# Kernel optimization log

Hardware: AMD Instinct MI355X
Metric: run time of the kernel (lower is better)

The kernel has to match this reference:

```python
import jax, jax.numpy as jnp
import numpy as np

N, NODE_DIM, EDGE_DIM, E, H, L, G = 100000, 128, 16, 1200000, 64, 3, 1000


def gcn_conv(x, w, b, row, col, dis):
    # PyG GCNConv: x @ W, symmetric-normalized aggregation with self-loops, + bias
    xw = x @ w                                    # [N, H]
    norm = dis[row] * dis[col]                    # [E]
    msg = norm[:, None] * xw[row]                 # [E, H]
    out = jax.ops.segment_sum(msg, col, num_segments=N)
    out = out + (dis * dis)[:, None] * xw         # self-loop contribution
    return out + b


def reference(x, edge_attr, node_w, node_b, edge_w, edge_b, conv_w, conv_b,
              cls_w1, cls_b1, cls_w2, cls_b2, edge_index, batch, num_graphs):
    row, col = edge_index[0], edge_index[1]
    # node embed
    h = x @ node_w + node_b                       # [N, H]
    # edge embed aggregated to both endpoints
    e = edge_attr @ edge_w + edge_b               # [E, H]
    edge_aggr = jax.ops.segment_sum(e, row, num_segments=N) \
              + jax.ops.segment_sum(e, col, num_segments=N)
    h = h + edge_aggr
    # degree with self-loops (deg over col, matching PyG GCNConv default flow)
    deg = jax.ops.segment_sum(jnp.ones((E,), h.dtype), col, num_segments=N) + 1.0
    dis = jnp.where(deg > 0, jax.lax.rsqrt(deg), 0.0)
    xs = []
    for i in range(L):
        h = jax.nn.relu(gcn_conv(h, conv_w[i], conv_b[i], row, col, dis))
        xs.append(h)
    hj = jnp.concatenate(xs, axis=-1)             # JumpingKnowledge 'cat' -> [N, L*H]
    # global mean pool over batch index
    sums = jax.ops.segment_sum(hj, batch, num_segments=num_graphs)
    cnts = jax.ops.segment_sum(jnp.ones((N,), hj.dtype), batch, num_segments=num_graphs)
    pooled = sums / jnp.maximum(cnts, 1.0)[:, None]  # [G, L*H]
    # classifier (eval mode: dropout is identity)
    z = jax.nn.relu(pooled @ cls_w1 + cls_b1)
    out = z @ cls_w2 + cls_b2                     # [G, 1]
    return out.squeeze(-1)


def setup_inputs() -> dict:
    key = jax.random.key(0)
    ks = jax.random.split(key, 16)
    s = lambda fan: 1.0 / np.sqrt(fan)
    return {
        "x": jax.random.normal(ks[0], (N, NODE_DIM), jnp.float32),
        "edge_attr": jax.random.normal(ks[1], (E, EDGE_DIM), jnp.float32),
        "node_w": jax.random.uniform(ks[2], (NODE_DIM, H), jnp.float32, -s(NODE_DIM), s(NODE_DIM)),
        "node_b": jnp.zeros((H,), jnp.float32),
        "edge_w": jax.random.uniform(ks[3], (EDGE_DIM, H), jnp.float32, -s(EDGE_DIM), s(EDGE_DIM)),
        "edge_b": jnp.zeros((H,), jnp.float32),
        "conv_w": jax.random.uniform(ks[4], (L, H, H), jnp.float32, -s(H), s(H)),
        "conv_b": jnp.zeros((L, H), jnp.float32),
        "cls_w1": jax.random.uniform(ks[5], (L * H, H // 2), jnp.float32, -s(L * H), s(L * H)),
        "cls_b1": jnp.zeros((H // 2,), jnp.float32),
        "cls_w2": jax.random.uniform(ks[6], (H // 2, 1), jnp.float32, -s(H // 2), s(H // 2)),
        "cls_b2": jnp.zeros((1,), jnp.float32),
        "edge_index": jax.random.randint(ks[7], (2, E), 0, N, jnp.int64 if jax.config.jax_enable_x64 else jnp.int32),
        "batch": jnp.sort(jax.random.randint(ks[8], (N,), 0, G, jnp.int64 if jax.config.jax_enable_x64 else jnp.int32)),
        "num_graphs": G,
    }
```

## Files before the change

kernel.cpp:

```cpp
#include <hip/hip_runtime.h>
#include <math.h>


#define EPB 4096

__global__ __launch_bounds__(256) void k_embed(
    const float* __restrict__ x, const float* __restrict__ w,
    const float* __restrict__ b, float* __restrict__ out, int N) {
  __shared__ __align__(16) float rl[64 * 128];
  const int t = threadIdx.x;
  const int j = t & 63;
  const int wv = t >> 6;
  const int base = blockIdx.x * 64;
  float wr[128];
#pragma unroll
  for (int k = 0; k < 128; ++k) wr[k] = w[k * 64 + j];
  const float bj = b[j];
#pragma unroll
  for (int it = 0; it < 8; ++it) {
    int lin = (t + it * 256) * 4;
    int r = lin >> 7, c = lin & 127;
    int row = base + r;
    float4 v = (row < N) ? *(const float4*)&x[(size_t)row * 128 + c]
                         : make_float4(0.f, 0.f, 0.f, 0.f);
    *(float4*)&rl[lin] = v;
  }
  __syncthreads();
  for (int r = wv; r < 64; r += 4) {
    int row = base + r;
    if (row >= N) break;
    float acc = bj;
#pragma unroll
    for (int k4 = 0; k4 < 32; ++k4) {
      float4 a = *(const float4*)&rl[r * 128 + k4 * 4];
      acc = fmaf(a.x, wr[k4 * 4 + 0], acc);
      acc = fmaf(a.y, wr[k4 * 4 + 1], acc);
      acc = fmaf(a.z, wr[k4 * 4 + 2], acc);
      acc = fmaf(a.w, wr[k4 * 4 + 3], acc);
    }
    out[(size_t)row * 64 + j] = acc;
  }
}

__global__ __launch_bounds__(256) void k_conv(
    const float* __restrict__ hin, const float* __restrict__ w,
    const float* __restrict__ dis, float* __restrict__ xws, int N) {
  __shared__ __align__(16) float rl[64 * 64];
  const int t = threadIdx.x;
  const int j = t & 63;
  const int wv = t >> 6;
  const int base = blockIdx.x * 64;
  float wr[64];
#pragma unroll
  for (int k = 0; k < 64; ++k) wr[k] = w[k * 64 + j];
#pragma unroll
  for (int it = 0; it < 4; ++it) {
    int lin = (t + it * 256) * 4;
    int r = lin >> 6, c = lin & 63;
    int row = base + r;
    float4 v = (row < N) ? *(const float4*)&hin[(size_t)row * 64 + c]
                         : make_float4(0.f, 0.f, 0.f, 0.f);
    *(float4*)&rl[lin] = v;
  }
  __syncthreads();
  for (int r = wv; r < 64; r += 4) {
    int row = base + r;
    if (row >= N) break;
    float acc = 0.f;
#pragma unroll
    for (int k4 = 0; k4 < 16; ++k4) {
      float4 a = *(const float4*)&rl[r * 64 + k4 * 4];
      acc = fmaf(a.x, wr[k4 * 4 + 0], acc);
      acc = fmaf(a.y, wr[k4 * 4 + 1], acc);
      acc = fmaf(a.z, wr[k4 * 4 + 2], acc);
      acc = fmaf(a.w, wr[k4 * 4 + 3], acc);
    }
    xws[(size_t)row * 64 + j] = dis[row] * acc;
  }
}

__global__ __launch_bounds__(256) void k_hist(
    const int* __restrict__ erow, const int* __restrict__ ecol,
    int* __restrict__ matTc, int* __restrict__ matTr, int E, int NB, int NBLK) {
  __shared__ int hc[512], hr[512];
  int b = blockIdx.x, t = threadIdx.x;
  for (int i = t; i < NB; i += 256) { hc[i] = 0; hr[i] = 0; }
  __syncthreads();
  int e0 = b * EPB;
#pragma unroll
  for (int q = 0; q < 16; ++q) {
    int e = e0 + q * 256 + t;
    if (e < E) {
      atomicAdd(&hc[ecol[e] >> 8], 1);
      atomicAdd(&hr[erow[e] >> 8], 1);
    }
  }
  __syncthreads();
  for (int i = t; i < NB; i += 256) {
    matTc[(size_t)i * NBLK + b] = hc[i];
    matTr[(size_t)i * NBLK + b] = hr[i];
  }
}

__global__ __launch_bounds__(256) void kBscan(
    int* __restrict__ matTc, int* __restrict__ matTr,
    int* __restrict__ totc, int* __restrict__ totr, int NB, int NBLK) {
  __shared__ int sc[256];
  int bi = blockIdx.x, t = threadIdx.x;
  int side = (bi >= NB) ? 1 : 0;
  int i = bi - side * NB;
  int* row = (side ? matTr : matTc) + (size_t)i * NBLK;
  int* tot = side ? totr : totc;
  int e0 = (2 * t < NBLK) ? row[2 * t] : 0;
  int e1 = (2 * t + 1 < NBLK) ? row[2 * t + 1] : 0;
  int s = e0 + e1;
  sc[t] = s;
  __syncthreads();
  for (int d = 1; d < 256; d <<= 1) {
    int x = (t >= d) ? sc[t - d] : 0;
    __syncthreads();
    sc[t] += x;
    __syncthreads();
  }
  int excl = sc[t] - s;
  if (2 * t < NBLK) row[2 * t] = excl;
  if (2 * t + 1 < NBLK) row[2 * t + 1] = excl + e0;
  if (t == 255) tot[i] = sc[255];
}

__global__ __launch_bounds__(512) void kB2(
    const int* __restrict__ totc, const int* __restrict__ totr,
    int* __restrict__ startc, int* __restrict__ startr, int NB) {
  __shared__ int sc[512];
  int t = threadIdx.x;
  const int* tot = blockIdx.x ? totr : totc;
  int* start = blockIdx.x ? startr : startc;
  int s = (t < NB) ? tot[t] : 0;
  sc[t] = s;
  __syncthreads();
  for (int d = 1; d < 512; d <<= 1) {
    int x = (t >= d) ? sc[t - d] : 0;
    __syncthreads();
    sc[t] += x;
    __syncthreads();
  }
  if (t < NB) start[t] = sc[t] - s;
}

__global__ __launch_bounds__(256) void k_scat(
    const int* __restrict__ erow, const int* __restrict__ ecol,
    const int* __restrict__ matTc, const int* __restrict__ matTr,
    const int* __restrict__ startc, const int* __restrict__ startr,
    unsigned long long* __restrict__ tmpc, unsigned int* __restrict__ tmpr,
    int E, int NB, int NBLK) {
  __shared__ int curc[512], curr[512];
  int b = blockIdx.x, t = threadIdx.x;
  for (int i = t; i < NB; i += 256) {
    curc[i] = startc[i] + matTc[(size_t)i * NBLK + b];
    curr[i] = startr[i] + matTr[(size_t)i * NBLK + b];
  }
  __syncthreads();
  int e0 = b * EPB;
#pragma unroll
  for (int q = 0; q < 16; ++q) {
    int e = e0 + q * 256 + t;
    if (e < E) {
      int r = erow[e], c = ecol[e];
      int pc = atomicAdd(&curc[c >> 8], 1);
      tmpc[pc] = (unsigned long long)(c & 255) |
                 ((unsigned long long)r << 8) |
                 ((unsigned long long)e << 25);
      int pr = atomicAdd(&curr[r >> 8], 1);
      tmpr[pr] = ((unsigned int)e << 8) | (unsigned int)(r & 255);
    }
  }
}

__global__ __launch_bounds__(256) void k_bcount(
    const unsigned long long* __restrict__ tmpc,
    const unsigned int* __restrict__ tmpr,
    const int* __restrict__ startc, const int* __restrict__ startr,
    const int* __restrict__ totc, const int* __restrict__ totr,
    int* __restrict__ indeg, int* __restrict__ outdeg,
    int* __restrict__ offc, int* __restrict__ offr, int N, int NB) {
  __shared__ int h[256], sc[256];
  int bi = blockIdx.x, t = threadIdx.x;
  int side = (bi >= NB) ? 1 : 0;
  int b = bi - side * NB;
  h[t] = 0;
  __syncthreads();
  int bstart = side ? startr[b] : startc[b];
  int cnt = side ? totr[b] : totc[b];
  if (side) {
    for (int i = t; i < cnt; i += 256)
      atomicAdd(&h[(int)(tmpr[bstart + i] & 255)], 1);
  } else {
    for (int i = t; i < cnt; i += 256)
      atomicAdd(&h[(int)(tmpc[bstart + i] & 255)], 1);
  }
  __syncthreads();
  int s = h[t];
  sc[t] = s;
  __syncthreads();
  for (int d = 1; d < 256; d <<= 1) {
    int x = (t >= d) ? sc[t - d] : 0;
    __syncthreads();
    sc[t] += x;
    __syncthreads();
  }
  int n = (b << 8) + t;
  if (n < N) {
    if (side) { outdeg[n] = s; offr[n] = bstart + sc[t] - s; }
    else      { indeg[n] = s;  offc[n] = bstart + sc[t] - s; }
  }
}

__global__ __launch_bounds__(256) void k_place(
    const unsigned long long* __restrict__ tmpc,
    const unsigned int* __restrict__ tmpr,
    const int* __restrict__ offc, const int* __restrict__ offr,
    int* __restrict__ srcl, int* __restrict__ eidc, int* __restrict__ eidr,
    int N, int E, int NB) {
  __shared__ int cur[256];
  int bi = blockIdx.x, t = threadIdx.x;
  int side = (bi >= NB) ? 1 : 0;
  int b = bi - side * NB;
  const int* off = side ? offr : offc;
  int nodebase = b << 8;
  int nb = min(256, N - nodebase);
  if (t < nb) cur[t] = off[nodebase + t];
  __syncthreads();
  int bstart = off[nodebase];
  int bend = (nodebase + 256 < N) ? off[nodebase + 256] : E;
  if (side) {
    for (int idx = bstart + t; idx < bend; idx += 256) {
      unsigned int v = tmpr[idx];
      int p = atomicAdd(&cur[(int)(v & 255)], 1);
      eidr[p] = (int)(v >> 8);
    }
  } else {
    for (int idx = bstart + t; idx < bend; idx += 256) {
      unsigned long long v = tmpc[idx];
      int p = atomicAdd(&cur[(int)(v & 255)], 1);
      srcl[p] = (int)((v >> 8) & 0x1FFFF);
      eidc[p] = (int)(v >> 25);
    }
  }
}

__global__ __launch_bounds__(256) void k_eembed(
    const float* __restrict__ ea, const int* __restrict__ eidc,
    const int* __restrict__ eidr, const int* __restrict__ offc,
    const int* __restrict__ indeg, const int* __restrict__ offr,
    const int* __restrict__ outdeg, const float* __restrict__ ew,
    const float* __restrict__ eb, float* h0, float* __restrict__ dis, int N) {
  int t = blockIdx.x * 256 + threadIdx.x;
  int n = __builtin_amdgcn_readfirstlane(t >> 6);
  if (n >= N) return;
  int lane = threadIdx.x & 63;
  int slot = lane >> 4, kk = lane & 15;
  int cin = indeg[n], basec = offc[n];
  int cout = outdeg[n], baser = offr[n];
  float acc = 0.f;
  int c0 = (cin > 0) ? cin - 1 : 0;
  for (int i = 0; i < cin; i += 32) {
#pragma unroll
    for (int q = 0; q < 8; ++q) {
      int idx = i + q * 4 + slot;
      int eid = eidc[basec + min(idx, c0)];
      float v = ea[(size_t)eid * 16 + kk];
      acc += (idx < cin) ? v : 0.f;
    }
  }
  int r0 = (cout > 0) ? cout - 1 : 0;
  for (int i = 0; i < cout; i += 32) {
#pragma unroll
    for (int q = 0; q < 8; ++q) {
      int idx = i + q * 4 + slot;
      int eid = eidr[baser + min(idx, r0)];
      float v = ea[(size_t)eid * 16 + kk];
      acc += (idx < cout) ? v : 0.f;
    }
  }
  acc += __shfl_xor(acc, 16, 64);
  acc += __shfl_xor(acc, 32, 64);
  int j = lane;
  float v = h0[(size_t)n * 64 + j] + (float)(cin + cout) * eb[j];
#pragma unroll
  for (int k = 0; k < 16; ++k) {
    float ak = __shfl(acc, k, 64);
    v = fmaf(ak, ew[k * 64 + j], v);
  }
  h0[(size_t)n * 64 + j] = v;
  if (j == 0) dis[n] = 1.0f / sqrtf((float)cin + 1.0f);
}

__global__ __launch_bounds__(256) void k_gather(
    const float* __restrict__ xws, const float* __restrict__ dis,
    const int* __restrict__ offc, const int* __restrict__ indeg,
    const int* __restrict__ srcl, const float* __restrict__ b,
    float* __restrict__ h0, float* __restrict__ hj_slice, int N) {
  const int t = threadIdx.x;
  const int lane = t & 63;
  const int s = lane >> 4;
  const int fg = lane & 15;
  int n = blockIdx.x * 16 + (t >> 6) * 4 + s;
  bool ok = (n < N);
  int nn = ok ? n : (N - 1);
  int cnt = indeg[nn];
  int boff = offc[nn];
  int c0 = (cnt > 0) ? cnt - 1 : 0;
  float4 acc = *(const float4*)&xws[(size_t)nn * 64 + fg * 4];
  for (int i = 0; i < cnt; i += 8) {
    float4 v[8];
#pragma unroll
    for (int q = 0; q < 8; ++q) {
      int src = srcl[boff + min(i + q, c0)];
      v[q] = *(const float4*)&xws[(size_t)src * 64 + fg * 4];
    }
#pragma unroll
    for (int q = 0; q < 8; ++q) {
      if (i + q < cnt) {
        acc.x += v[q].x; acc.y += v[q].y; acc.z += v[q].z; acc.w += v[q].w;
      }
    }
  }
  float d = dis[nn];
  float4 bb = *(const float4*)&b[fg * 4];
  float4 act;
  act.x = fmaxf(fmaf(d, acc.x, bb.x), 0.f);
  act.y = fmaxf(fmaf(d, acc.y, bb.y), 0.f);
  act.z = fmaxf(fmaf(d, acc.z, bb.z), 0.f);
  act.w = fmaxf(fmaf(d, acc.w, bb.w), 0.f);
  if (ok) {
    if (h0 != nullptr) *(float4*)&h0[(size_t)n * 64 + fg * 4] = act;
    *(float4*)&hj_slice[(size_t)n * 192 + fg * 4] = act;
  }
}

__global__ __launch_bounds__(192) void k_pool(
    const float* __restrict__ hj, const int* __restrict__ batch, int N,
    const float* __restrict__ w1, const float* __restrict__ b1,
    const float* __restrict__ w2, const float* __restrict__ b2,
    float* __restrict__ out) {
  __shared__ float pl[192];
  int g = blockIdx.x;
  int t = threadIdx.x;
  int lo = 0, hi = N;
  while (lo < hi) { int m = (lo + hi) >> 1; if (batch[m] < g) lo = m + 1; else hi = m; }
  int start = lo;
  hi = N;
  while (lo < hi) { int m = (lo + hi) >> 1; if (batch[m] < g + 1) lo = m + 1; else hi = m; }
  int end = lo;
  float s = 0.f;
  for (int r = start; r < end; ++r) s += hj[(size_t)r * 192 + t];
  int cnt = end - start;
  pl[t] = s / (float)(cnt > 0 ? cnt : 1);
  __syncthreads();
  if (t < 64) {
    float val = 0.f;
    if (t < 32) {
      float z = b1[t];
#pragma unroll 8
      for (int k = 0; k < 192; ++k) z = fmaf(pl[k], w1[k * 32 + t], z);
      z = fmaxf(z, 0.f);
      val = z * w2[t];
    }
#pragma unroll
    for (int off = 16; off > 0; off >>= 1) val += __shfl_down(val, off);
    if (t == 0) out[g] = val + b2[0];
  }
}

extern "C" void kernel_launch(void* const* d_in, const int* in_sizes, int n_in,
                              void* d_out, int out_size, void* d_ws, size_t ws_size,
                              hipStream_t stream) {
  const float* x      = (const float*)d_in[0];
  const float* ea     = (const float*)d_in[1];
  const float* node_w = (const float*)d_in[2];
  const float* node_b = (const float*)d_in[3];
  const float* edge_w = (const float*)d_in[4];
  const float* edge_b = (const float*)d_in[5];
  const float* conv_w = (const float*)d_in[6];
  const float* conv_b = (const float*)d_in[7];
  const float* w1     = (const float*)d_in[8];
  const float* b1     = (const float*)d_in[9];
  const float* w2     = (const float*)d_in[10];
  const float* b2     = (const float*)d_in[11];
  const int*   ei     = (const int*)d_in[12];
  const int*   batch  = (const int*)d_in[13];

  const int N = in_sizes[0] / 128;
  const int E = in_sizes[12] / 2;
  const int G = out_size;
  const int* erow = ei;
  const int* ecol = ei + E;

  float* ws = (float*)d_ws;
  size_t o = 0;
  float* h0    = ws + o; o += (size_t)N * 64;
  float* xws   = ws + o; o += (size_t)N * 64;
  float* hj    = ws + o; o += (size_t)N * 192;
  float* dis   = ws + o; o += N;
  int* indeg   = (int*)(ws + o); o += N;
  int* outdeg  = (int*)(ws + o); o += N;
  int* offc    = (int*)(ws + o); o += N;
  int* offr    = (int*)(ws + o); o += N;
  int* srcl    = (int*)(ws + o); o += E;
  int* eidc    = (int*)(ws + o); o += E;
  int* eidr    = (int*)(ws + o); o += E;

  const int NB = (N + 255) >> 8;
  const int NBLK = (E + EPB - 1) / EPB;
  unsigned long long* tmpc = (unsigned long long*)hj;
  unsigned int* tmpr = (unsigned int*)(hj + (size_t)2 * E);
  int* matTc = (int*)(hj + (size_t)3 * E);
  int* matTr = matTc + (size_t)NB * NBLK;
  int* totc  = matTr + (size_t)NB * NBLK;
  int* startc = totc + NB;
  int* totr  = startc + NB;
  int* startr = totr + NB;
  float* out = (float*)d_out;

  dim3 b256(256);
  const int NT = (N + 63) / 64;

  k_embed<<<NT, b256, 0, stream>>>(x, node_w, node_b, h0, N);
  k_hist<<<NBLK, b256, 0, stream>>>(erow, ecol, matTc, matTr, E, NB, NBLK);
  kBscan<<<2 * NB, b256, 0, stream>>>(matTc, matTr, totc, totr, NB, NBLK);
  kB2<<<2, dim3(512), 0, stream>>>(totc, totr, startc, startr, NB);
  k_scat<<<NBLK, b256, 0, stream>>>(erow, ecol, matTc, matTr, startc, startr,
                                    tmpc, tmpr, E, NB, NBLK);
  k_bcount<<<2 * NB, b256, 0, stream>>>(tmpc, tmpr, startc, startr, totc, totr,
                                        indeg, outdeg, offc, offr, N, NB);
  k_place<<<2 * NB, b256, 0, stream>>>(tmpc, tmpr, offc, offr,
                                       srcl, eidc, eidr, N, E, NB);
  k_eembed<<<((size_t)N * 64 + 255) / 256, b256, 0, stream>>>(
      ea, eidc, eidr, offc, indeg, offr, outdeg, edge_w, edge_b, h0, dis, N);
  for (int l = 0; l < 3; ++l) {
    k_conv<<<NT, b256, 0, stream>>>(
        h0, conv_w + (size_t)l * 64 * 64, dis, xws, N);
    k_gather<<<(N + 15) / 16, b256, 0, stream>>>(
        xws, dis, offc, indeg, srcl, conv_b + (size_t)l * 64,
        (l < 2) ? h0 : nullptr, hj + (size_t)l * 64, N);
  }
  k_pool<<<G, dim3(192), 0, stream>>>(hj, batch, N, w1, b1, w2, b2, out);
}
```

Before: 457.3 us.

## Fuse next-layer GEMM into gather epilogue and merge bucket count/place kernels

The gather kernel for each GCN layer now also computes the next layer's x@W product scaled by dis, from activations staged in LDS. This removes the separate conv kernels for layers 2 and 3 along with the h0 write and reread, and ping-pongs between two xws buffers. It also merges the bucket count/scan and placement kernels into one, reusing the shared prefix sums as placement cursors so offsets are not reread from global memory. The cost is a 64-register weight preload, a block-wide sync in each gather block, and an extra N×64 workspace buffer.

```diff
diff --git a/kernel.cpp b/kernel.cpp
--- a/kernel.cpp
+++ b/kernel.cpp
@@ -176,13 +176,15 @@
   }
 }
 
-__global__ __launch_bounds__(256) void k_bcount(
+__global__ __launch_bounds__(256) void k_bplace(
     const unsigned long long* __restrict__ tmpc,
     const unsigned int* __restrict__ tmpr,
     const int* __restrict__ startc, const int* __restrict__ startr,
     const int* __restrict__ totc, const int* __restrict__ totr,
     int* __restrict__ indeg, int* __restrict__ outdeg,
-    int* __restrict__ offc, int* __restrict__ offr, int N, int NB) {
+    int* __restrict__ offc, int* __restrict__ offr,
+    int* __restrict__ srcl, int* __restrict__ eidc, int* __restrict__ eidr,
+    int N, int NB) {
   __shared__ int h[256], sc[256];
   int bi = blockIdx.x, t = threadIdx.x;
   int side = (bi >= NB) ? 1 : 0;
@@ -209,39 +211,23 @@
     __syncthreads();
   }
   int n = (b << 8) + t;
+  int myoff = bstart + sc[t] - s;
   if (n < N) {
-    if (side) { outdeg[n] = s; offr[n] = bstart + sc[t] - s; }
-    else      { indeg[n] = s;  offc[n] = bstart + sc[t] - s; }
-  }
-}
-
-__global__ __launch_bounds__(256) void k_place(
-    const unsigned long long* __restrict__ tmpc,
-    const unsigned int* __restrict__ tmpr,
-    const int* __restrict__ offc, const int* __restrict__ offr,
-    int* __restrict__ srcl, int* __restrict__ eidc, int* __restrict__ eidr,
-    int N, int E, int NB) {
-  __shared__ int cur[256];
-  int bi = blockIdx.x, t = threadIdx.x;
-  int side = (bi >= NB) ? 1 : 0;
-  int b = bi - side * NB;
-  const int* off = side ? offr : offc;
-  int nodebase = b << 8;
-  int nb = min(256, N - nodebase);
-  if (t < nb) cur[t] = off[nodebase + t];
-  __syncthreads();
-  int bstart = off[nodebase];
-  int bend = (nodebase + 256 < N) ? off[nodebase + 256] : E;
+    if (side) { outdeg[n] = s; offr[n] = myoff; }
+    else      { indeg[n] = s;  offc[n] = myoff; }
+  }
+  h[t] = myoff;
+  __syncthreads();
   if (side) {
-    for (int idx = bstart + t; idx < bend; idx += 256) {
-      unsigned int v = tmpr[idx];
-      int p = atomicAdd(&cur[(int)(v & 255)], 1);
+    for (int i = t; i < cnt; i += 256) {
+      unsigned int v = tmpr[bstart + i];
+      int p = atomicAdd(&h[(int)(v & 255)], 1);
       eidr[p] = (int)(v >> 8);
     }
   } else {
-    for (int idx = bstart + t; idx < bend; idx += 256) {
-      unsigned long long v = tmpc[idx];
-      int p = atomicAdd(&cur[(int)(v & 255)], 1);
+    for (int i = t; i < cnt; i += 256) {
+      unsigned long long v = tmpc[bstart + i];
+      int p = atomicAdd(&h[(int)(v & 255)], 1);
       srcl[p] = (int)((v >> 8) & 0x1FFFF);
       eidc[p] = (int)(v >> 25);
     }
@@ -295,28 +281,34 @@
   if (j == 0) dis[n] = 1.0f / sqrtf((float)cin + 1.0f);
 }
 
-__global__ __launch_bounds__(256) void k_gather(
-    const float* __restrict__ xws, const float* __restrict__ dis,
+__global__ __launch_bounds__(256) void k_gc(
+    const float* __restrict__ xin, const float* __restrict__ dis,
     const int* __restrict__ offc, const int* __restrict__ indeg,
-    const int* __restrict__ srcl, const float* __restrict__ b,
-    float* __restrict__ h0, float* __restrict__ hj_slice, int N) {
+    const int* __restrict__ srcl, const float* __restrict__ bprev,
+    const float* __restrict__ wnext, float* __restrict__ hj_slice,
+    float* __restrict__ xout, int N) {
+  __shared__ __align__(16) float act_lds[16][64];
+  __shared__ float disl[16];
   const int t = threadIdx.x;
   const int lane = t & 63;
   const int s = lane >> 4;
   const int fg = lane & 15;
-  int n = blockIdx.x * 16 + (t >> 6) * 4 + s;
+  const int nb = blockIdx.x * 16;
+  const int wid = t >> 6;
+  const int li = wid * 4 + s;
+  int n = nb + li;
   bool ok = (n < N);
   int nn = ok ? n : (N - 1);
   int cnt = indeg[nn];
   int boff = offc[nn];
   int c0 = (cnt > 0) ? cnt - 1 : 0;
-  float4 acc = *(const float4*)&xws[(size_t)nn * 64 + fg * 4];
+  float4 acc = *(const float4*)&xin[(size_t)nn * 64 + fg * 4];
   for (int i = 0; i < cnt; i += 8) {
     float4 v[8];
 #pragma unroll
     for (int q = 0; q < 8; ++q) {
       int src = srcl[boff + min(i + q, c0)];
-      v[q] = *(const float4*)&xws[(size_t)src * 64 + fg * 4];
+      v[q] = *(const float4*)&xin[(size_t)src * 64 + fg * 4];
     }
 #pragma unroll
     for (int q = 0; q < 8; ++q) {
@@ -326,15 +318,35 @@
     }
   }
   float d = dis[nn];
-  float4 bb = *(const float4*)&b[fg * 4];
+  float4 bb = *(const float4*)&bprev[fg * 4];
   float4 act;
   act.x = fmaxf(fmaf(d, acc.x, bb.x), 0.f);
   act.y = fmaxf(fmaf(d, acc.y, bb.y), 0.f);
   act.z = fmaxf(fmaf(d, acc.z, bb.z), 0.f);
   act.w = fmaxf(fmaf(d, acc.w, bb.w), 0.f);
-  if (ok) {
-    if (h0 != nullptr) *(float4*)&h0[(size_t)n * 64 + fg * 4] = act;
-    *(float4*)&hj_slice[(size_t)n * 192 + fg * 4] = act;
+  if (ok) *(float4*)&hj_slice[(size_t)n * 192 + fg * 4] = act;
+  *(float4*)&act_lds[li][fg * 4] = act;
+  if (fg == 0) disl[li] = d;
+  if (wnext == nullptr) return;
+  __syncthreads();
+  float wr[64];
+#pragma unroll
+  for (int k = 0; k < 64; ++k) wr[k] = wnext[k * 64 + lane];
+#pragma unroll
+  for (int q = 0; q < 4; ++q) {
+    int li2 = wid * 4 + q;
+    int n2 = nb + li2;
+    if (n2 >= N) break;
+    float a = 0.f;
+#pragma unroll
+    for (int k4 = 0; k4 < 16; ++k4) {
+      float4 av = *(const float4*)&act_lds[li2][k4 * 4];
+      a = fmaf(av.x, wr[k4 * 4 + 0], a);
+      a = fmaf(av.y, wr[k4 * 4 + 1], a);
+      a = fmaf(av.z, wr[k4 * 4 + 2], a);
+      a = fmaf(av.w, wr[k4 * 4 + 3], a);
+    }
+    xout[(size_t)n2 * 64 + lane] = disl[li2] * a;
   }
 }
 
@@ -399,7 +411,8 @@
   float* ws = (float*)d_ws;
   size_t o = 0;
   float* h0    = ws + o; o += (size_t)N * 64;
-  float* xws   = ws + o; o += (size_t)N * 64;
+  float* xwsA  = ws + o; o += (size_t)N * 64;
+  float* xwsB  = ws + o; o += (size_t)N * 64;
   float* hj    = ws + o; o += (size_t)N * 192;
   float* dis   = ws + o; o += N;
   int* indeg   = (int*)(ws + o); o += N;
@@ -431,18 +444,20 @@
   kB2<<<2, dim3(512), 0, stream>>>(totc, totr, startc, startr, NB);
   k_scat<<<NBLK, b256, 0, stream>>>(erow, ecol, matTc, matTr, startc, startr,
                                     tmpc, tmpr, E, NB, NBLK);
-  k_bcount<<<2 * NB, b256, 0, stream>>>(tmpc, tmpr, startc, startr, totc, totr,
-                                        indeg, outdeg, offc, offr, N, NB);
-  k_place<<<2 * NB, b256, 0, stream>>>(tmpc, tmpr, offc, offr,
-                                       srcl, eidc, eidr, N, E, NB);
+  k_bplace<<<2 * NB, b256, 0, stream>>>(tmpc, tmpr, startc, startr, totc, totr,
+                                        indeg, outdeg, offc, offr,
+                                        srcl, eidc, eidr, N, NB);
   k_eembed<<<((size_t)N * 64 + 255) / 256, b256, 0, stream>>>(
       ea, eidc, eidr, offc, indeg, offr, outdeg, edge_w, edge_b, h0, dis, N);
-  for (int l = 0; l < 3; ++l) {
-    k_conv<<<NT, b256, 0, stream>>>(
-        h0, conv_w + (size_t)l * 64 * 64, dis, xws, N);
-    k_gather<<<(N + 15) / 16, b256, 0, stream>>>(
-        xws, dis, offc, indeg, srcl, conv_b + (size_t)l * 64,
-        (l < 2) ? h0 : nullptr, hj + (size_t)l * 64, N);
-  }
+  k_conv<<<NT, b256, 0, stream>>>(h0, conv_w, dis, xwsA, N);
+  k_gc<<<(N + 15) / 16, b256, 0, stream>>>(
+      xwsA, dis, offc, indeg, srcl, conv_b,
+      conv_w + (size_t)1 * 64 * 64, hj, xwsB, N);
+  k_gc<<<(N + 15) / 16, b256, 0, stream>>>(
+      xwsB, dis, offc, indeg, srcl, conv_b + 64,
+      conv_w + (size_t)2 * 64 * 64, hj + 64, xwsA, N);
+  k_gc<<<(N + 15) / 16, b256, 0, stream>>>(
+      xwsA, dis, offc, indeg, srcl, conv_b + 128,
+      nullptr, hj + 128, nullptr, N);
   k_pool<<<G, dim3(192), 0, stream>>>(hj, batch, N, w1, b1, w2, b2, out);
 }
```

Result: faster. 441.7 us (-3.4%).
